# Optimization experiments

Measured on AMD Instinct MI355X. Metric: run time of the kernel, lower is better.

## Reference

```python
import jax, jax.numpy as jnp
import numpy as np
from jax import lax

EPROJS, DUNITS, ATT_DIM = 512, 1024, 320
ACONV_CHANS, ACONV_FILTS = 10, 100
B, T = 64, 2048
SCALING = 2.0


def setup_inputs() -> dict:
    key = jax.random.key(0)
    ks = jax.random.split(key, 10)
    enc_hs_pad = jax.random.normal(ks[0], (B, T, EPROJS), dtype=jnp.float32)
    # lengths in [T//2, T] so no row is fully masked
    enc_hs_len = jax.random.randint(ks[1], (B,), T // 2, T + 1).astype(jnp.int32)
    dec_z = jax.random.normal(ks[2], (B, DUNITS), dtype=jnp.float32)
    att_prev = jax.random.uniform(ks[3], (B, T), dtype=jnp.float32)
    # normalize att_prev like a prob. distribution over valid frames
    att_prev = att_prev / jnp.sum(att_prev, axis=1, keepdims=True)
    s = 0.02
    W_enc = jax.random.normal(ks[4], (ATT_DIM, EPROJS), dtype=jnp.float32) * s
    b_enc = jnp.zeros((ATT_DIM,), dtype=jnp.float32)
    W_dec = jax.random.normal(ks[5], (ATT_DIM, DUNITS), dtype=jnp.float32) * s
    W_att = jax.random.normal(ks[6], (ATT_DIM, ACONV_CHANS), dtype=jnp.float32) * s
    # Conv2d(1, aconv_chans, (1, 2*filts+1)) acts as 1D conv over time
    conv_w = jax.random.normal(ks[7], (ACONV_CHANS, 1, 2 * ACONV_FILTS + 1), dtype=jnp.float32) * s
    W_g = jax.random.normal(ks[8], (1, ATT_DIM), dtype=jnp.float32) * s
    b_g = jnp.zeros((1,), dtype=jnp.float32)
    return {
        "enc_hs_pad": enc_hs_pad, "enc_hs_len": enc_hs_len, "dec_z": dec_z,
        "att_prev": att_prev, "W_enc": W_enc, "b_enc": b_enc, "W_dec": W_dec,
        "W_att": W_att, "conv_w": conv_w, "W_g": W_g, "b_g": b_g,
    }


def reference(enc_hs_pad, enc_hs_len, dec_z, att_prev,
              W_enc, b_enc, W_dec, W_att, conv_w, W_g, b_g):
    # pre_compute_enc_h = mlp_enc(enc_h): [B, T, att_dim]
    pre_enc = jnp.einsum('bte,ae->bta', enc_hs_pad, W_enc) + b_enc
    # location conv: att_prev [B, T] -> [B, C, T] (SAME padding)
    att_conv = lax.conv_general_dilated(
        att_prev[:, None, :], conv_w, window_strides=(1,),
        padding=[(ACONV_FILTS, ACONV_FILTS)],
        dimension_numbers=('NCH', 'OIH', 'NCH'))
    # mlp_att over channels: [B, T, att_dim]
    att_feat = jnp.einsum('bct,ac->bta', att_conv, W_att)
    # mlp_dec(dec_z): [B, 1, att_dim]
    dec_feat = (dec_z @ W_dec.T)[:, None, :]
    # energies: gvec(tanh(sum)) -> [B, T]
    e = jnp.einsum('bta,a->bt', jnp.tanh(att_feat + pre_enc + dec_feat), W_g[0]) + b_g[0]
    # mask padded frames
    t_idx = jnp.arange(e.shape[1])
    pad_mask = t_idx[None, :] >= enc_hs_len[:, None]
    e = jnp.where(pad_mask, -jnp.inf, e)
    w = jax.nn.softmax(SCALING * e, axis=1)
    # context: weighted sum over encoder states -> [B, D_enc]
    c = jnp.einsum('bte,bt->be', enc_hs_pad, w)
    return (c, w)
```

## Files before the change

kernel.cpp:

```cpp
#include <hip/hip_runtime.h>
#include <hip/hip_bf16.h>

#define B_SZ 64
#define T_SZ 2048
#define EPROJS 512
#define DUNITS 1024
#define ATT_DIM 320
#define NCH 10
#define KFILT 201
#define PAD 100

typedef __attribute__((ext_vector_type(8))) __bf16 bf16x8;
typedef __attribute__((ext_vector_type(4))) float f32x4;
typedef __attribute__((ext_vector_type(8))) unsigned short u16x8;

__device__ __forceinline__ unsigned short f2b(float f) {
    __bf16 h = (__bf16)f;
    return __builtin_bit_cast(unsigned short, h);
}

__global__ void front_k(const float* __restrict__ W_enc, unsigned short* __restrict__ wbf,
                        const float* __restrict__ dec_z, const float* __restrict__ W_dec,
                        const float* __restrict__ b_enc, float* __restrict__ df,
                        const float* __restrict__ ap, const float* __restrict__ cw,
                        float* __restrict__ conv_out)
{
    __shared__ float s_ap[T_SZ];
    __shared__ float s_cw[KFILT];
    int blk = blockIdx.x, tid = threadIdx.x;

    if (blk < 160) {
        int i = (blk * 256 + tid) * 4;
        float4 v = *(const float4*)(W_enc + i);
        ushort4 o;
        o.x = f2b(v.x); o.y = f2b(v.y); o.z = f2b(v.z); o.w = f2b(v.w);
        *(ushort4*)(wbf + i) = o;
    } else if (blk < 240) {
        int idx = (blk - 160) * 256 + tid;
        int b = idx / ATT_DIM, a = idx - b * ATT_DIM;
        const float4* z = (const float4*)(dec_z + b * DUNITS);
        const float4* w = (const float4*)(W_dec + (size_t)a * DUNITS);
        float s = b_enc[a];
        #pragma unroll 4
        for (int d = 0; d < DUNITS / 4; ++d) {
            float4 zv = z[d], wv = w[d];
            s += zv.x * wv.x + zv.y * wv.y + zv.z * wv.z + zv.w * wv.w;
        }
        df[b * ATT_DIM + a] = s;
    } else {
        int cb = blk - 240;
        int b = cb / NCH, c = cb - b * NCH;
        for (int i = tid; i < T_SZ; i += 256) s_ap[i] = ap[b * T_SZ + i];
        for (int i = tid; i < KFILT; i += 256) s_cw[i] = cw[c * KFILT + i];
        __syncthreads();
        for (int j = 0; j < T_SZ / 256; ++j) {
            int t = tid + j * 256;
            int klo = max(0, PAD - t);
            int khi = min(KFILT, T_SZ + PAD - t);
            float s = 0.f;
            for (int k = klo; k < khi; ++k) s += s_ap[t - PAD + k] * s_cw[k];
            conv_out[((size_t)(b * NCH + c)) * T_SZ + t] = s;
        }
    }
}

__global__ __launch_bounds__(512, 1) void energy_k(
    const float* __restrict__ enc, const unsigned short* __restrict__ wbf,
    const float* __restrict__ df, const float* __restrict__ att_conv,
    const float* __restrict__ W_att, const float* __restrict__ W_g,
    const int* __restrict__ len, float* __restrict__ e_out)
{
    __shared__ unsigned short sW[2][1280 * 8];
    __shared__ float sDf[ATT_DIM], sWg[ATT_DIM], sWatt[ATT_DIM * NCH], sConv[NCH * 128];

    int tid = threadIdx.x;
    int lane = tid & 63, wave = tid >> 6;
    int b = blockIdx.x >> 4;
    int t0 = (blockIdx.x & 15) << 7;

    if (t0 >= len[b]) return;

    int m15 = lane & 15, kg = lane >> 4;
    int row = t0 + wave * 16 + m15;
    const float* aP = enc + ((size_t)b * T_SZ + row) * EPROJS;

    int q0 = tid >> 6;        int g0 = (q0 * 205) >> 10; int wr0 = tid - g0 * 320;
    int i1 = tid + 512;  int q1 = i1 >> 6; int g1 = (q1 * 205) >> 10; int wr1 = i1 - g1 * 320;
    int i2 = tid + 1024; int q2 = i2 >> 6; int g2 = (q2 * 205) >> 10; int wr2 = i2 - g2 * 320;
    bool do2 = tid < 256;
    const unsigned short* wp0 = wbf + (size_t)wr0 * EPROJS + g0 * 8;
    const unsigned short* wp1 = wbf + (size_t)wr1 * EPROJS + g1 * 8;
    const unsigned short* wp2 = wbf + (size_t)wr2 * EPROJS + g2 * 8;

    {
        u16x8 v0 = *(const u16x8*)wp0;
        u16x8 v1 = *(const u16x8*)wp1;
        *(u16x8*)(&sW[0][tid * 8]) = v0;
        *(u16x8*)(&sW[0][i1 * 8]) = v1;
        if (do2) {
            u16x8 v2 = *(const u16x8*)wp2;
            *(u16x8*)(&sW[0][i2 * 8]) = v2;
        }
    }
    float4 a0 = *(const float4*)(aP + kg * 8);
    float4 a1 = *(const float4*)(aP + kg * 8 + 4);

    for (int i = tid; i < ATT_DIM; i += 512) { sDf[i] = df[b * ATT_DIM + i]; sWg[i] = W_g[i]; }
    for (int i = tid; i < ATT_DIM * NCH; i += 512) sWatt[i] = W_att[i];
    for (int i = tid; i < NCH * 128; i += 512)
        sConv[i] = att_conv[((size_t)(b * NCH + (i >> 7))) * T_SZ + t0 + (i & 127)];

    f32x4 acc[20];
    #pragma unroll
    for (int n = 0; n < 20; ++n) acc[n] = (f32x4){0.f, 0.f, 0.f, 0.f};

    __syncthreads();

    for (int t = 0; t < 16; ++t) {
        int cur = t & 1;
        int kn = ((t + 1) & 15) * 32;
        u16x8 w0 = *(const u16x8*)(wp0 + kn);
        u16x8 w1 = *(const u16x8*)(wp1 + kn);
        u16x8 w2;
        if (do2) w2 = *(const u16x8*)(wp2 + kn);
        float4 n0 = *(const float4*)(aP + kn + kg * 8);
        float4 n1 = *(const float4*)(aP + kn + kg * 8 + 4);

        bf16x8 af;
        af[0] = (__bf16)a0.x; af[1] = (__bf16)a0.y; af[2] = (__bf16)a0.z; af[3] = (__bf16)a0.w;
        af[4] = (__bf16)a1.x; af[5] = (__bf16)a1.y; af[6] = (__bf16)a1.z; af[7] = (__bf16)a1.w;
        const unsigned short* sw = sW[cur];
        #pragma unroll
        for (int nt = 0; nt < 20; ++nt) {
            int wr = nt * 16 + m15;
            bf16x8 wf = *(const bf16x8*)(sw + (kg * 320 + wr) * 8);
            acc[nt] = __builtin_amdgcn_mfma_f32_16x16x32_bf16(af, wf, acc[nt], 0, 0, 0);
        }

        unsigned short* swn = (unsigned short*)sW[cur ^ 1];
        *(u16x8*)(&swn[tid * 8]) = w0;
        *(u16x8*)(&swn[i1 * 8]) = w1;
        if (do2) *(u16x8*)(&swn[i2 * 8]) = w2;
        a0 = n0; a1 = n1;

        asm volatile("s_waitcnt lgkmcnt(0)" ::: "memory");
        __builtin_amdgcn_s_barrier();
    }

    int tl_base = wave * 16 + kg * 4;
    #pragma unroll
    for (int r = 0; r < 4; ++r) {
        int tl = tl_base + r;
        float s = 0.f;
        #pragma unroll
        for (int nt = 0; nt < 20; ++nt) {
            int col = nt * 16 + m15;
            float v = acc[nt][r] + sDf[col];
            float afeat = 0.f;
            #pragma unroll
            for (int c = 0; c < NCH; ++c) afeat += sWatt[col * NCH + c] * sConv[c * 128 + tl];
            v += afeat;
            v = fminf(fmaxf(v, -15.f), 15.f);
            float e2 = __expf(2.f * v);
            s += sWg[col] * ((e2 - 1.f) / (e2 + 1.f));
        }
        s += __shfl_xor(s, 1); s += __shfl_xor(s, 2);
        s += __shfl_xor(s, 4); s += __shfl_xor(s, 8);
        if (m15 == 0) e_out[b * T_SZ + t0 + tl] = s;
    }
}

__global__ void softmax_ctx_k(const float* __restrict__ e, const int* __restrict__ len,
                              const float* __restrict__ enc,
                              float* __restrict__ w_out, float* __restrict__ part) {
    int b = blockIdx.x, tc = blockIdx.y, tid = threadIdx.x;
    int lane = tid & 63, wave = tid >> 6;
    int L = len[b];
    int tb = tc * 128;
    int half = tid >> 7;
    int c4 = tid & 127;
    float* po = part + ((size_t)(b * 32 + tc * 2 + half)) * EPROJS + c4 * 4;

    if (tb >= L) {
        if (tid < 128) w_out[b * T_SZ + tb + tid] = 0.f;
        *(f32x4*)po = (f32x4){0.f, 0.f, 0.f, 0.f};
        return;
    }

    float ev[8];
    float m = -1e30f;
    #pragma unroll
    for (int i = 0; i < 8; ++i) {
        int t = tid + i * 256;
        float x = e[b * T_SZ + t];
        if (t >= L) x = -1e30f;
        ev[i] = x;
        m = fmaxf(m, x);
    }
    #pragma unroll
    for (int o = 32; o > 0; o >>= 1) m = fmaxf(m, __shfl_xor(m, o));
    __shared__ float sred[4];
    if (lane == 0) sred[wave] = m;
    __syncthreads();
    m = fmaxf(fmaxf(sred[0], sred[1]), fmaxf(sred[2], sred[3]));

    float sum = 0.f;
    #pragma unroll
    for (int i = 0; i < 8; ++i) sum += __expf(2.f * (ev[i] - m));
    #pragma unroll
    for (int o = 32; o > 0; o >>= 1) sum += __shfl_xor(sum, o);
    __shared__ float sred2[4];
    if (lane == 0) sred2[wave] = sum;
    __syncthreads();
    sum = sred2[0] + sred2[1] + sred2[2] + sred2[3];
    float inv = 1.f / sum;

    if (tid < 128) {
        int t = tb + tid;
        float wv = 0.f;
        if (t < L) wv = __expf(2.f * (e[b * T_SZ + t] - m)) * inv;
        w_out[b * T_SZ + t] = wv;
    }

    f32x4 s = (f32x4){0.f, 0.f, 0.f, 0.f};
    #pragma unroll 4
    for (int i = half; i < 128; i += 2) {
        int t = tb + i;
        float ee = e[b * T_SZ + t];
        float wv = (t < L) ? __expf(2.f * (ee - m)) * inv : 0.f;
        f32x4 v = *(const f32x4*)(enc + ((size_t)b * T_SZ + t) * EPROJS + c4 * 4);
        s += wv * v;
    }
    *(f32x4*)po = s;
}

__global__ void ctx_reduce_k(const float* __restrict__ part, float* __restrict__ c_out) {
    int b = blockIdx.x;
    int c4 = threadIdx.x;
    f32x4 s = (f32x4){0.f, 0.f, 0.f, 0.f};
    #pragma unroll
    for (int tc = 0; tc < 32; ++tc)
        s += *(const f32x4*)(part + ((size_t)(b * 32 + tc)) * EPROJS + c4 * 4);
    *(f32x4*)(c_out + b * EPROJS + c4 * 4) = s;
}

extern "C" void kernel_launch(void* const* d_in, const int* in_sizes, int n_in,
                              void* d_out, int out_size, void* d_ws, size_t ws_size,
                              hipStream_t stream) {
    const float* enc      = (const float*)d_in[0];
    const int*   len      = (const int*)d_in[1];
    const float* dec_z    = (const float*)d_in[2];
    const float* att_prev = (const float*)d_in[3];
    const float* W_enc    = (const float*)d_in[4];
    const float* b_enc    = (const float*)d_in[5];
    const float* W_dec    = (const float*)d_in[6];
    const float* W_att    = (const float*)d_in[7];
    const float* conv_w   = (const float*)d_in[8];
    const float* W_g      = (const float*)d_in[9];

    char* ws = (char*)d_ws;
    size_t off = 0;
    unsigned short* wbf = (unsigned short*)(ws + off); off += (size_t)ATT_DIM * EPROJS * 2;
    float* e_buf  = (float*)(ws + off); off += (size_t)B_SZ * T_SZ * 4;
    float* dfb    = (float*)(ws + off); off += (size_t)B_SZ * ATT_DIM * 4;
    float* att_cv = (float*)(ws + off); off += (size_t)B_SZ * NCH * T_SZ * 4;
    float* part   = (float*)(ws + off); off += (size_t)B_SZ * 32 * EPROJS * 4;

    float* c_out = (float*)d_out;
    float* w_out = (float*)d_out + B_SZ * EPROJS;

    front_k<<<dim3(880), dim3(256), 0, stream>>>(W_enc, wbf, dec_z, W_dec, b_enc, dfb,
                                                 att_prev, conv_w, att_cv);
    energy_k<<<dim3(B_SZ * 16), dim3(512), 0, stream>>>(enc, wbf, dfb, att_cv, W_att, W_g, len, e_buf);
    softmax_ctx_k<<<dim3(B_SZ, 16), dim3(256), 0, stream>>>(e_buf, len, enc, w_out, part);
    ctx_reduce_k<<<dim3(B_SZ), dim3(128), 0, stream>>>(part, c_out);
}
```

Measured before the change: 206.8 us.

## Swap energy GEMM operand roles: stage encoder tile in LDS, stream weights per wave

The energy kernel now stages the 128-row encoder tile, converted to bf16, in double-buffered LDS. Each of 10 waves reads its own 32-column slice of W_enc directly from global memory, where before the full weight matrix was staged in LDS. This cuts LDS footprint and accumulator registers so that two 640-thread blocks can share a CU. The epilogue then needs a cross-wave shared-memory reduction of the energies, and the per-wave weight loads come straight from global/L2 with no prefetch ahead of use.

```diff
diff --git a/kernel.cpp b/kernel.cpp
--- a/kernel.cpp
+++ b/kernel.cpp
@@ -64,14 +64,15 @@
     }
 }
 
-__global__ __launch_bounds__(512, 1) void energy_k(
+__global__ __launch_bounds__(640, 2) void energy_k(
     const float* __restrict__ enc, const unsigned short* __restrict__ wbf,
     const float* __restrict__ df, const float* __restrict__ att_conv,
     const float* __restrict__ W_att, const float* __restrict__ W_g,
     const int* __restrict__ len, float* __restrict__ e_out)
 {
-    __shared__ unsigned short sW[2][1280 * 8];
+    __shared__ unsigned short sEnc[2][512 * 8];
     __shared__ float sDf[ATT_DIM], sWg[ATT_DIM], sWatt[ATT_DIM * NCH], sConv[NCH * 128];
+    __shared__ float sE[10][128];
 
     int tid = threadIdx.x;
     int lane = tid & 63, wave = tid >> 6;
@@ -81,92 +82,93 @@
     if (t0 >= len[b]) return;
 
     int m15 = lane & 15, kg = lane >> 4;
-    int row = t0 + wave * 16 + m15;
-    const float* aP = enc + ((size_t)b * T_SZ + row) * EPROJS;
-
-    int q0 = tid >> 6;        int g0 = (q0 * 205) >> 10; int wr0 = tid - g0 * 320;
-    int i1 = tid + 512;  int q1 = i1 >> 6; int g1 = (q1 * 205) >> 10; int wr1 = i1 - g1 * 320;
-    int i2 = tid + 1024; int q2 = i2 >> 6; int g2 = (q2 * 205) >> 10; int wr2 = i2 - g2 * 320;
-    bool do2 = tid < 256;
-    const unsigned short* wp0 = wbf + (size_t)wr0 * EPROJS + g0 * 8;
-    const unsigned short* wp1 = wbf + (size_t)wr1 * EPROJS + g1 * 8;
-    const unsigned short* wp2 = wbf + (size_t)wr2 * EPROJS + g2 * 8;
-
-    {
-        u16x8 v0 = *(const u16x8*)wp0;
-        u16x8 v1 = *(const u16x8*)wp1;
-        *(u16x8*)(&sW[0][tid * 8]) = v0;
-        *(u16x8*)(&sW[0][i1 * 8]) = v1;
-        if (do2) {
-            u16x8 v2 = *(const u16x8*)wp2;
-            *(u16x8*)(&sW[0][i2 * 8]) = v2;
-        }
-    }
-    float4 a0 = *(const float4*)(aP + kg * 8);
-    float4 a1 = *(const float4*)(aP + kg * 8 + 4);
-
-    for (int i = tid; i < ATT_DIM; i += 512) { sDf[i] = df[b * ATT_DIM + i]; sWg[i] = W_g[i]; }
-    for (int i = tid; i < ATT_DIM * NCH; i += 512) sWatt[i] = W_att[i];
-    for (int i = tid; i < NCH * 128; i += 512)
+    const unsigned short* wq0 = wbf + (size_t)(wave * 32 + m15) * EPROJS + kg * 8;
+    const unsigned short* wq1 = wq0 + 16 * EPROJS;
+
+    bool doStage = tid < 512;
+    int srow = tid & 127, sg = tid >> 7;
+    const float* sp = enc + ((size_t)b * T_SZ + t0 + srow) * EPROJS + sg * 8;
+
+    if (doStage) {
+        float4 f0 = *(const float4*)(sp);
+        float4 f1 = *(const float4*)(sp + 4);
+        u16x8 v;
+        v[0] = f2b(f0.x); v[1] = f2b(f0.y); v[2] = f2b(f0.z); v[3] = f2b(f0.w);
+        v[4] = f2b(f1.x); v[5] = f2b(f1.y); v[6] = f2b(f1.z); v[7] = f2b(f1.w);
+        *(u16x8*)(&sEnc[0][tid * 8]) = v;
+    }
+
+    for (int i = tid; i < ATT_DIM; i += 640) { sDf[i] = df[b * ATT_DIM + i]; sWg[i] = W_g[i]; }
+    for (int i = tid; i < ATT_DIM * NCH; i += 640) sWatt[i] = W_att[i];
+    for (int i = tid; i < NCH * 128; i += 640)
         sConv[i] = att_conv[((size_t)(b * NCH + (i >> 7))) * T_SZ + t0 + (i & 127)];
 
-    f32x4 acc[20];
-    #pragma unroll
-    for (int n = 0; n < 20; ++n) acc[n] = (f32x4){0.f, 0.f, 0.f, 0.f};
+    f32x4 acc[16];
+    #pragma unroll
+    for (int n = 0; n < 16; ++n) acc[n] = (f32x4){0.f, 0.f, 0.f, 0.f};
 
     __syncthreads();
 
     for (int t = 0; t < 16; ++t) {
         int cur = t & 1;
+        int k0 = t * 32;
         int kn = ((t + 1) & 15) * 32;
-        u16x8 w0 = *(const u16x8*)(wp0 + kn);
-        u16x8 w1 = *(const u16x8*)(wp1 + kn);
-        u16x8 w2;
-        if (do2) w2 = *(const u16x8*)(wp2 + kn);
-        float4 n0 = *(const float4*)(aP + kn + kg * 8);
-        float4 n1 = *(const float4*)(aP + kn + kg * 8 + 4);
-
-        bf16x8 af;
-        af[0] = (__bf16)a0.x; af[1] = (__bf16)a0.y; af[2] = (__bf16)a0.z; af[3] = (__bf16)a0.w;
-        af[4] = (__bf16)a1.x; af[5] = (__bf16)a1.y; af[6] = (__bf16)a1.z; af[7] = (__bf16)a1.w;
-        const unsigned short* sw = sW[cur];
+
+        float4 f0, f1;
+        if (doStage) {
+            f0 = *(const float4*)(sp + kn);
+            f1 = *(const float4*)(sp + kn + 4);
+        }
+        bf16x8 wa0 = *(const bf16x8*)(wq0 + k0);
+        bf16x8 wa1 = *(const bf16x8*)(wq1 + k0);
+
+        const unsigned short* se = sEnc[cur];
         #pragma unroll
-        for (int nt = 0; nt < 20; ++nt) {
-            int wr = nt * 16 + m15;
-            bf16x8 wf = *(const bf16x8*)(sw + (kg * 320 + wr) * 8);
-            acc[nt] = __builtin_amdgcn_mfma_f32_16x16x32_bf16(af, wf, acc[nt], 0, 0, 0);
-        }
-
-        unsigned short* swn = (unsigned short*)sW[cur ^ 1];
-        *(u16x8*)(&swn[tid * 8]) = w0;
-        *(u16x8*)(&swn[i1 * 8]) = w1;
-        if (do2) *(u16x8*)(&swn[i2 * 8]) = w2;
-        a0 = n0; a1 = n1;
+        for (int nt = 0; nt < 8; ++nt) {
+            bf16x8 bf = *(const bf16x8*)(se + ((kg << 7) + nt * 16 + m15) * 8);
+            acc[nt]     = __builtin_amdgcn_mfma_f32_16x16x32_bf16(wa0, bf, acc[nt],     0, 0, 0);
+            acc[8 + nt] = __builtin_amdgcn_mfma_f32_16x16x32_bf16(wa1, bf, acc[8 + nt], 0, 0, 0);
+        }
+
+        if (doStage) {
+            u16x8 v;
+            v[0] = f2b(f0.x); v[1] = f2b(f0.y); v[2] = f2b(f0.z); v[3] = f2b(f0.w);
+            v[4] = f2b(f1.x); v[5] = f2b(f1.y); v[6] = f2b(f1.z); v[7] = f2b(f1.w);
+            *(u16x8*)(&sEnc[cur ^ 1][tid * 8]) = v;
+        }
 
         asm volatile("s_waitcnt lgkmcnt(0)" ::: "memory");
         __builtin_amdgcn_s_barrier();
     }
 
-    int tl_base = wave * 16 + kg * 4;
-    #pragma unroll
-    for (int r = 0; r < 4; ++r) {
-        int tl = tl_base + r;
+    #pragma unroll
+    for (int nt = 0; nt < 8; ++nt) {
+        int tl = nt * 16 + m15;
         float s = 0.f;
         #pragma unroll
-        for (int nt = 0; nt < 20; ++nt) {
-            int col = nt * 16 + m15;
-            float v = acc[nt][r] + sDf[col];
-            float afeat = 0.f;
+        for (int mt = 0; mt < 2; ++mt) {
             #pragma unroll
-            for (int c = 0; c < NCH; ++c) afeat += sWatt[col * NCH + c] * sConv[c * 128 + tl];
-            v += afeat;
-            v = fminf(fmaxf(v, -15.f), 15.f);
-            float e2 = __expf(2.f * v);
-            s += sWg[col] * ((e2 - 1.f) / (e2 + 1.f));
-        }
-        s += __shfl_xor(s, 1); s += __shfl_xor(s, 2);
-        s += __shfl_xor(s, 4); s += __shfl_xor(s, 8);
-        if (m15 == 0) e_out[b * T_SZ + t0 + tl] = s;
+            for (int r = 0; r < 4; ++r) {
+                int att = wave * 32 + mt * 16 + kg * 4 + r;
+                float v = acc[mt * 8 + nt][r] + sDf[att];
+                float afeat = 0.f;
+                #pragma unroll
+                for (int c = 0; c < NCH; ++c) afeat += sWatt[att * NCH + c] * sConv[c * 128 + tl];
+                v += afeat;
+                v = fminf(fmaxf(v, -15.f), 15.f);
+                float e2 = __expf(2.f * v);
+                s += sWg[att] * ((e2 - 1.f) / (e2 + 1.f));
+            }
+        }
+        s += __shfl_xor(s, 16); s += __shfl_xor(s, 32);
+        if (kg == 0) sE[wave][tl] = s;
+    }
+    __syncthreads();
+    if (tid < 128) {
+        float s = 0.f;
+        #pragma unroll
+        for (int w = 0; w < 10; ++w) s += sE[w][tid];
+        e_out[b * T_SZ + t0 + tid] = s;
     }
 }
 
@@ -271,7 +273,7 @@
 
     front_k<<<dim3(880), dim3(256), 0, stream>>>(W_enc, wbf, dec_z, W_dec, b_enc, dfb,
                                                  att_prev, conv_w, att_cv);
-    energy_k<<<dim3(B_SZ * 16), dim3(512), 0, stream>>>(enc, wbf, dfb, att_cv, W_att, W_g, len, e_buf);
+    energy_k<<<dim3(B_SZ * 16), dim3(640), 0, stream>>>(enc, wbf, dfb, att_cv, W_att, W_g, len, e_buf);
     softmax_ctx_k<<<dim3(B_SZ, 16), dim3(256), 0, stream>>>(e_buf, len, enc, w_out, part);
     ctx_reduce_k<<<dim3(B_SZ), dim3(128), 0, stream>>>(part, c_out);
 }
```

Result: slower. 244.9 us (+18.4%).
